# Optimization experiments

Hardware: AMD Instinct MI355X
Metric: run time of the kernel (lower is better)

Reference implementation:

```python
import jax, jax.numpy as jnp
import numpy as np

N, E, DIM, HEADS, EDGE_DIM = 50000, 800000, 128, 4, 1
C = DIM // HEADS  # per-head channels
EPS = 1e-5


def graph_ln(h, w, b):
    # PyG LayerNorm, mode='graph', batch=None: normalize over ALL nodes+features
    mu = h.mean()
    hc = h - mu
    std = jnp.sqrt(jnp.mean(hc * hc))
    return hc / (std + EPS) * w + b


def setup_inputs() -> dict:
    key = jax.random.key(0)
    ks = jax.random.split(key, 16)
    s = 1.0 / np.sqrt(DIM)
    return {
        "x": jax.random.normal(ks[0], (N, DIM), jnp.float32),
        "edge_index": jax.random.randint(ks[1], (2, E), 0, N, jnp.int32),
        "edge_weight": jax.random.uniform(ks[2], (E,), jnp.float32),
        "edge_attr": jax.random.normal(ks[3], (E, EDGE_DIM), jnp.float32),
        # GCNConv params
        "W_gcn": jax.random.normal(ks[4], (DIM, DIM), jnp.float32) * s,
        "b_gcn": jnp.zeros((DIM,), jnp.float32),
        # GATv2Conv params (share_weights=True -> single lin)
        "W_l": jax.random.normal(ks[5], (DIM, DIM), jnp.float32) * s,
        "b_l": jnp.zeros((DIM,), jnp.float32),
        "W_edge": jax.random.normal(ks[6], (EDGE_DIM, DIM), jnp.float32),
        "att": jax.random.normal(ks[7], (HEADS, C), jnp.float32) * (1.0 / np.sqrt(C)),
        "b_gat": jnp.zeros((DIM,), jnp.float32),
        # norms
        "gcn_nw": jnp.ones((DIM,), jnp.float32), "gcn_nb": jnp.zeros((DIM,), jnp.float32),
        "gat_nw": jnp.ones((DIM,), jnp.float32), "gat_nb": jnp.zeros((DIM,), jnp.float32),
        "out_nw": jnp.ones((DIM,), jnp.float32), "out_nb": jnp.zeros((DIM,), jnp.float32),
        "alpha": jnp.ones((2,), jnp.float32),
    }


def reference(x, edge_index, edge_weight, edge_attr, W_gcn, b_gcn, W_l, b_l,
              W_edge, att, b_gat, gcn_nw, gcn_nb, gat_nw, gat_nb, out_nw, out_nb, alpha):
    src, dst = edge_index[0], edge_index[1]

    # ---- GCN branch (normalize=True, add_self_loops=False) ----
    deg = jax.ops.segment_sum(edge_weight, dst, num_segments=N)
    dis = jnp.where(deg > 0, jax.lax.rsqrt(jnp.maximum(deg, 1e-30)), 0.0)
    norm = dis[src] * edge_weight * dis[dst]  # [E]
    xw = x @ W_gcn  # [N, DIM]
    h = jax.ops.segment_sum(norm[:, None] * xw[src], dst, num_segments=N) + b_gcn
    gcn_out = x + jax.nn.gelu(graph_ln(h, gcn_nw, gcn_nb), approximate=False)

    # ---- GATv2 branch (share_weights=True, edge_dim=1) ----
    xl = (x @ W_l + b_l).reshape(N, HEADS, C)
    e = (edge_attr @ W_edge).reshape(E, HEADS, C)
    z = jax.nn.leaky_relu(xl[dst] + xl[src] + e, negative_slope=0.2)  # [E,H,C]
    logits = jnp.einsum('ehc,hc->eh', z, att)  # [E,H]
    m = jax.ops.segment_max(logits, dst, num_segments=N)  # [N,H]
    a = jnp.exp(logits - m[dst])
    denom = jax.ops.segment_sum(a, dst, num_segments=N)
    a = a / (denom[dst] + 1e-16)  # softmax over incoming edges per dst, per head
    msg = xl[src] * a[:, :, None]  # [E,H,C]
    g = jax.ops.segment_sum(msg, dst, num_segments=N).reshape(N, DIM) + b_gat
    gat_out = x + jax.nn.gelu(graph_ln(g, gat_nw, gat_nb), approximate=False)

    # ---- fuse ----
    w = jax.nn.softmax(alpha)
    fused = w[0] * gcn_out + w[1] * gat_out
    return jax.nn.gelu(graph_ln(fused, out_nw, out_nb), approximate=False)
```

## Files before the change

kernel.cpp:

```cpp
#include <hip/hip_runtime.h>
#include <math.h>

#define DIM 128
#define HEADS 4
#define EPS 1e-5f
#define NBLK 1024

__device__ __forceinline__ float us2f(unsigned short u) {
  union { unsigned int i; float f; } c; c.i = ((unsigned int)u) << 16; return c.f;
}
__device__ __forceinline__ unsigned short f2us(float f) {
  union { float ff; unsigned int i; } c; c.ff = f;
  return (unsigned short)((c.i + 0x7FFFu + ((c.i >> 16) & 1u)) >> 16);
}
__device__ __forceinline__ float ldf(const void* p, size_t i, int fl32) {
  return fl32 ? ((const float*)p)[i] : us2f(((const unsigned short*)p)[i]);
}
__device__ __forceinline__ float gelu_exact(float v) {
  return 0.5f * v * (1.0f + erff(v * 0.7071067811865475f));
}
__device__ __forceinline__ int imin(int a, int b) { return a < b ? a : b; }

__device__ __forceinline__ int packed_pos(int c) { return ((c & ~1) << 1) | (c & 1); }

__global__ void __launch_bounds__(256)
k_detect(const unsigned short* __restrict__ x, long n, int* __restrict__ dflag) {
  long lim = n < 8192 ? n : 8192;
  int bad = 0;
  for (long i = threadIdx.x; i < lim; i += 256) {
    float v = us2f(x[i]);
    float a = fabsf(v);
    if (!(a == 0.0f || (a > 1e-30f && a < 1e3f))) bad++;
  }
  __shared__ int sb[256];
  sb[threadIdx.x] = bad;
  __syncthreads();
  for (int off = 128; off > 0; off >>= 1) {
    if ((int)threadIdx.x < off) sb[threadIdx.x] += sb[threadIdx.x + off];
    __syncthreads();
  }
  if (threadIdx.x == 0) dflag[0] = (sb[0] > 32) ? 1 : 0;
}

__global__ void k_deg_cnt(const int* __restrict__ dst, const void* __restrict__ ew,
                          float* __restrict__ deg, int* __restrict__ cnt,
                          int* __restrict__ rank, int E, const int* __restrict__ df) {
  const int fl32 = *df;
  int e = blockIdx.x * blockDim.x + threadIdx.x;
  if (e < E) {
    int d = dst[e];
    rank[e] = atomicAdd(&cnt[d], 1);
    float w = ldf(ew, e, fl32);
    if (isfinite(w)) atomicAdd(&deg[d], w);
  }
}

__global__ void k_dis(float* __restrict__ deg, int N) {
  int i = blockIdx.x * blockDim.x + threadIdx.x;
  if (i < N) {
    float d = deg[i];
    deg[i] = (d > 0.0f) ? rsqrtf(fmaxf(d, 1e-30f)) : 0.0f;
  }
}

__global__ void __launch_bounds__(256)
k_scan(const int* __restrict__ cnt, int* __restrict__ off, int N, int E) {
  __shared__ int part[256];
  int t = threadIdx.x;
  int chunk = (N + 255) / 256;
  int lo = t * chunk;
  int hi = lo + chunk; if (hi > N) hi = N;
  int s = 0;
  for (int i = lo; i < hi; ++i) s += cnt[i];
  part[t] = s;
  __syncthreads();
  if (t == 0) {
    int run = 0;
    for (int j = 0; j < 256; ++j) { int tmp = part[j]; part[j] = run; run += tmp; }
  }
  __syncthreads();
  int run = part[t];
  for (int i = lo; i < hi; ++i) { off[i] = run; run += cnt[i]; }
  if (t == 0) off[N] = E;
}

__global__ void k_scatter(const int* __restrict__ src, const int* __restrict__ dst,
                          const void* __restrict__ ew, const void* __restrict__ ea,
                          const float* __restrict__ dis, const int* __restrict__ off,
                          const int* __restrict__ rank, int4* __restrict__ csr,
                          int E, const int* __restrict__ df) {
  const int fl32 = *df;
  int e = blockIdx.x * blockDim.x + threadIdx.x;
  if (e >= E) return;
  int d = dst[e], s = src[e];
  int pos = off[d] + rank[e];
  float nm = dis[s] * ldf(ew, e, fl32) * dis[d];
  if (!isfinite(nm)) nm = 0.0f;
  float eav = ldf(ea, e, fl32);
  if (!isfinite(eav)) eav = 0.0f;
  csr[pos] = make_int4(s, __float_as_int(nm), __float_as_int(eav), 0);
}

__global__ void __launch_bounds__(256)
k_wprep(const void* __restrict__ Wg, const void* __restrict__ Wl,
        const void* __restrict__ bl, unsigned short* __restrict__ Bhi,
        unsigned short* __restrict__ Blo, float* __restrict__ bias2,
        const int* __restrict__ df) {
  const int fl32 = *df;
  int g = blockIdx.x * 256 + threadIdx.x;
  int col = g >> 7, k = g & 127;
  int t4 = col >> 2, r = col & 3;
  int wcol = t4 * 2 + (r & 1);
  float v = (r < 2) ? ldf(Wl, (size_t)k * DIM + wcol, fl32)
                    : ldf(Wg, (size_t)k * DIM + wcol, fl32);
  unsigned short hi = f2us(v);
  float lo = v - us2f(hi);
  Bhi[(size_t)col * 128 + k] = hi;
  Blo[(size_t)col * 128 + k] = f2us(lo);
  if (blockIdx.x == 0) {
    int c2 = threadIdx.x;
    int tt = c2 >> 2, rr = c2 & 3;
    bias2[c2] = (rr < 2) ? ldf(bl, tt * 2 + rr, fl32) : 0.0f;
  }
}

typedef __attribute__((ext_vector_type(8))) short short8v;
typedef __attribute__((ext_vector_type(4))) float f32x4;

__global__ void __launch_bounds__(256)
k_gemm_mfma(const void* __restrict__ x, const unsigned short* __restrict__ Bhi,
            const unsigned short* __restrict__ Blo, const float* __restrict__ bias2,
            unsigned short* __restrict__ packed, int N, const int* __restrict__ df) {
  const int fl32 = *df;
  __shared__ unsigned short Ahi[64 * 128];
  __shared__ unsigned short Alo[64 * 128];
  const int tid = threadIdx.x;
  const int r0 = blockIdx.x * 64;
  #pragma unroll
  for (int it = 0; it < 8; ++it) {
    int i4 = tid + it * 256;
    int row = i4 >> 5, kq = i4 & 31;
    int grow = r0 + row;
    float v0 = 0.f, v1 = 0.f, v2 = 0.f, v3 = 0.f;
    if (grow < N) {
      if (fl32) {
        float4 f = ((const float4*)x)[(size_t)grow * 32 + kq];
        v0 = f.x; v1 = f.y; v2 = f.z; v3 = f.w;
      } else {
        ushort4 u = ((const ushort4*)x)[(size_t)grow * 32 + kq];
        v0 = us2f(u.x); v1 = us2f(u.y); v2 = us2f(u.z); v3 = us2f(u.w);
      }
    }
    ushort4 hi = make_ushort4(f2us(v0), f2us(v1), f2us(v2), f2us(v3));
    ushort4 lo = make_ushort4(f2us(v0 - us2f(hi.x)), f2us(v1 - us2f(hi.y)),
                              f2us(v2 - us2f(hi.z)), f2us(v3 - us2f(hi.w)));
    int ba = (row * 256 + kq * 8) ^ ((row & 7) << 4);
    *(ushort4*)((char*)Ahi + ba) = hi;
    *(ushort4*)((char*)Alo + ba) = lo;
  }
  __syncthreads();
  const int lane = tid & 63, wid = tid >> 6;
  const int mbase = (wid >> 1) * 32;
  const int nbase = (wid & 1) * 128;
  const int lr = lane & 15, lk = lane >> 4;
  short8v ah[2][4], al[2][4];
  #pragma unroll
  for (int m = 0; m < 2; ++m) {
    #pragma unroll
    for (int ks = 0; ks < 4; ++ks) {
      int row = mbase + m * 16 + lr;
      int ba = (row * 256 + ks * 64 + lk * 16) ^ ((row & 7) << 4);
      ah[m][ks] = *(const short8v*)((const char*)Ahi + ba);
      al[m][ks] = *(const short8v*)((const char*)Alo + ba);
    }
  }
  f32x4 acc[2][8];
  const f32x4 zero = {0.0f, 0.0f, 0.0f, 0.0f};
  #pragma unroll
  for (int m = 0; m < 2; ++m)
    #pragma unroll
    for (int n = 0; n < 8; ++n) acc[m][n] = zero;
  #pragma unroll
  for (int n = 0; n < 8; ++n) {
    int col = nbase + n * 16 + lr;
    const unsigned short* bh0 = Bhi + (size_t)col * 128 + lk * 8;
    const unsigned short* bl0 = Blo + (size_t)col * 128 + lk * 8;
    #pragma unroll
    for (int ks = 0; ks < 4; ++ks) {
      short8v bh  = *(const short8v*)(bh0 + ks * 32);
      short8v blv = *(const short8v*)(bl0 + ks * 32);
      acc[0][n] = __builtin_amdgcn_mfma_f32_16x16x32_bf16(ah[0][ks], bh, acc[0][n], 0, 0, 0);
      acc[1][n] = __builtin_amdgcn_mfma_f32_16x16x32_bf16(ah[1][ks], bh, acc[1][n], 0, 0, 0);
      acc[0][n] = __builtin_amdgcn_mfma_f32_16x16x32_bf16(al[0][ks], bh, acc[0][n], 0, 0, 0);
      acc[1][n] = __builtin_amdgcn_mfma_f32_16x16x32_bf16(al[1][ks], bh, acc[1][n], 0, 0, 0);
      acc[0][n] = __builtin_amdgcn_mfma_f32_16x16x32_bf16(ah[0][ks], blv, acc[0][n], 0, 0, 0);
      acc[1][n] = __builtin_amdgcn_mfma_f32_16x16x32_bf16(ah[1][ks], blv, acc[1][n], 0, 0, 0);
    }
  }
  #pragma unroll
  for (int m = 0; m < 2; ++m) {
    #pragma unroll
    for (int n = 0; n < 8; ++n) {
      int col = nbase + n * 16 + lr;
      float bv = bias2[col];
      int rb = r0 + mbase + m * 16 + lk * 4;
      #pragma unroll
      for (int j = 0; j < 4; ++j) {
        int row = rb + j;
        if (row < N) {
          float v = acc[m][n][j] + bv;
          if (!isfinite(v)) v = 0.0f;
          packed[(size_t)row * 256 + col] = f2us(v);
        }
      }
    }
  }
}

#define GATHER(sidx) (*(const ushort4*)(packed + (size_t)(sidx) * 256 + lane * 4))

#define PROC(v, m) {                                                       \
  float nm = __int_as_float((m).y), eav = __int_as_float((m).z);           \
  float vx = us2f((v).x), vy = us2f((v).y);                                \
  float z0 = xd0 + vx + eav * wd0; z0 = (z0 > 0.f) ? z0 : 0.2f * z0;       \
  float z1 = xd1 + vy + eav * wd1; z1 = (z1 > 0.f) ? z1 : 0.2f * z1;       \
  float dt = z0 * at0 + z1 * at1;                                          \
  dt += __shfl_xor(dt, 1);                                                 \
  dt += __shfl_xor(dt, 2);                                                 \
  dt += __shfl_xor(dt, 4);                                                 \
  dt += __shfl_xor(dt, 8);                                                 \
  float e = __expf(-fabsf(dt - mx));                                       \
  bool up = dt > mx;                                                       \
  float corr = up ? e : 1.0f;                                              \
  float w = up ? 1.0f : e;                                                 \
  mx = up ? dt : mx;                                                       \
  den = fmaf(den, corr, w);                                                \
  ga0 = fmaf(ga0, corr, w * vx);                                           \
  ga1 = fmaf(ga1, corr, w * vy);                                           \
  hc0 = fmaf(nm, us2f((v).z), hc0);                                        \
  hc1 = fmaf(nm, us2f((v).w), hc1);                                        \
}

__global__ void __launch_bounds__(256)
k_mega(const int* __restrict__ off, const int4* __restrict__ csr,
       const unsigned short* __restrict__ packed,
       const void* __restrict__ Wed, const void* __restrict__ att,
       const void* __restrict__ bgcn, const void* __restrict__ bgat,
       float* __restrict__ h, float* __restrict__ g,
       double* __restrict__ pA, double* __restrict__ pB, int N,
       const int* __restrict__ df) {
  const int fl32 = *df;
  const int wid = threadIdx.x >> 6;
  const int lane = threadIdx.x & 63;
  const int n0 = blockIdx.x * 4;
  const int node = n0 + wid;
  const int c0 = lane * 2;
  float wd0 = ldf(Wed, c0, fl32), wd1 = ldf(Wed, c0 + 1, fl32);
  float at0 = ldf(att, c0, fl32), at1 = ldf(att, c0 + 1, fl32);

  const int blkBeg = off[n0];
  const int nTop = (n0 + 4 < N) ? (n0 + 4) : N;
  const int blkEnd = off[nTop];

  int beg = 0, end = 0;
  float xd0 = 0.f, xd1 = 0.f;
  if (node < N) {
    beg = off[node]; end = off[node + 1];
    ushort4 xd = *(const ushort4*)(packed + (size_t)node * 256 + lane * 4);
    xd0 = us2f(xd.x); xd1 = us2f(xd.y);
  }
  float mx = -INFINITY, den = 0.f;
  float ga0 = 0.f, ga1 = 0.f, hc0 = 0.f, hc1 = 0.f;

  __shared__ int4 smeta[256];

  for (int base = blkBeg; base < blkEnd; base += 256) {
    int wlen = blkEnd - base; if (wlen > 256) wlen = 256;
    __syncthreads();
    if ((int)threadIdx.x < wlen) smeta[threadIdx.x] = csr[base + (int)threadIdx.x];
    __syncthreads();
    int lo = beg > base ? beg : base;
    int hiEnd = base + wlen;
    int hi = end < hiEnd ? end : hiEnd;
    int cnt = hi - lo;
    if (cnt > 0) {
      int s0 = lo - base;
      int last = s0 + cnt - 1;
      ushort4 v0, v1, v2, v3, v4, v5, v6, v7;
      v0 = GATHER(smeta[imin(s0 + 0, last)].x);
      v1 = GATHER(smeta[imin(s0 + 1, last)].x);
      v2 = GATHER(smeta[imin(s0 + 2, last)].x);
      v3 = GATHER(smeta[imin(s0 + 3, last)].x);
      v4 = GATHER(smeta[imin(s0 + 4, last)].x);
      v5 = GATHER(smeta[imin(s0 + 5, last)].x);
      v6 = GATHER(smeta[imin(s0 + 6, last)].x);
      v7 = GATHER(smeta[imin(s0 + 7, last)].x);
      int i = 0;
      for (; i + 8 <= cnt; i += 8) {
        int4 m;
        m = smeta[s0 + i + 0]; PROC(v0, m); v0 = GATHER(smeta[imin(s0 + i + 8,  last)].x);
        m = smeta[s0 + i + 1]; PROC(v1, m); v1 = GATHER(smeta[imin(s0 + i + 9,  last)].x);
        m = smeta[s0 + i + 2]; PROC(v2, m); v2 = GATHER(smeta[imin(s0 + i + 10, last)].x);
        m = smeta[s0 + i + 3]; PROC(v3, m); v3 = GATHER(smeta[imin(s0 + i + 11, last)].x);
        m = smeta[s0 + i + 4]; PROC(v4, m); v4 = GATHER(smeta[imin(s0 + i + 12, last)].x);
        m = smeta[s0 + i + 5]; PROC(v5, m); v5 = GATHER(smeta[imin(s0 + i + 13, last)].x);
        m = smeta[s0 + i + 6]; PROC(v6, m); v6 = GATHER(smeta[imin(s0 + i + 14, last)].x);
        m = smeta[s0 + i + 7]; PROC(v7, m); v7 = GATHER(smeta[imin(s0 + i + 15, last)].x);
      }
      if (i < cnt) { int4 m = smeta[s0 + i]; PROC(v0, m); ++i; }
      if (i < cnt) { int4 m = smeta[s0 + i]; PROC(v1, m); ++i; }
      if (i < cnt) { int4 m = smeta[s0 + i]; PROC(v2, m); ++i; }
      if (i < cnt) { int4 m = smeta[s0 + i]; PROC(v3, m); ++i; }
      if (i < cnt) { int4 m = smeta[s0 + i]; PROC(v4, m); ++i; }
      if (i < cnt) { int4 m = smeta[s0 + i]; PROC(v5, m); ++i; }
      if (i < cnt) { int4 m = smeta[s0 + i]; PROC(v6, m); ++i; }
    }
  }

  double sA = 0.0, sA2 = 0.0, sB = 0.0, sB2 = 0.0;
  if (node < N) {
    float inv = (end > beg) ? 1.0f / (den + 1e-16f) : 0.0f;
    ga0 *= inv; ga1 *= inv;
    if (!isfinite(ga0)) ga0 = 0.0f;
    if (!isfinite(ga1)) ga1 = 0.0f;
    if (!isfinite(hc0)) hc0 = 0.0f;
    if (!isfinite(hc1)) hc1 = 0.0f;
    *(float2*)(h + (size_t)node * DIM + c0) = make_float2(hc0, hc1);
    *(float2*)(g + (size_t)node * DIM + c0) = make_float2(ga0, ga1);
    float hA0 = hc0 + ldf(bgcn, c0, fl32), hA1 = hc1 + ldf(bgcn, c0 + 1, fl32);
    float gB0 = ga0 + ldf(bgat, c0, fl32), gB1 = ga1 + ldf(bgat, c0 + 1, fl32);
    sA  = (double)hA0 + (double)hA1;
    sA2 = (double)hA0 * hA0 + (double)hA1 * hA1;
    sB  = (double)gB0 + (double)gB1;
    sB2 = (double)gB0 * gB0 + (double)gB1 * gB1;
  }
  __shared__ double l1[256], l2[256], l3[256], l4[256];
  l1[threadIdx.x] = sA; l2[threadIdx.x] = sA2; l3[threadIdx.x] = sB; l4[threadIdx.x] = sB2;
  __syncthreads();
  for (int o = 128; o > 0; o >>= 1) {
    if ((int)threadIdx.x < o) {
      l1[threadIdx.x] += l1[threadIdx.x + o];
      l2[threadIdx.x] += l2[threadIdx.x + o];
      l3[threadIdx.x] += l3[threadIdx.x + o];
      l4[threadIdx.x] += l4[threadIdx.x + o];
    }
    __syncthreads();
  }
  if (threadIdx.x == 0) {
    pA[2 * blockIdx.x] = l1[0]; pA[2 * blockIdx.x + 1] = l2[0];
    pB[2 * blockIdx.x] = l3[0]; pB[2 * blockIdx.x + 1] = l4[0];
  }
}

__device__ __forceinline__ void ln_params(double S, double S2, double M, float* mu_out, float* sc_out) {
  double mu = S / M;
  double v = S2 / M - mu * mu;
  if (!(v > 0.0)) v = 0.0;
  float fmu = (float)mu;
  float sc = 1.0f / ((float)sqrt(v) + EPS);
  if (!isfinite(fmu)) fmu = 0.0f;
  if (!isfinite(sc)) sc = 0.0f;
  *mu_out = fmu; *sc_out = sc;
}

__global__ void __launch_bounds__(256)
k_fin12(const double* __restrict__ pA, const double* __restrict__ pB, int nblk,
        const void* __restrict__ alpha, float* __restrict__ params, double M,
        const int* __restrict__ df) {
  const int fl32 = *df;
  __shared__ double l1[256], l2[256], l3[256], l4[256];
  double a = 0, b = 0, c = 0, d = 0;
  for (int j = threadIdx.x; j < nblk; j += 256) {
    a += pA[2 * j]; b += pA[2 * j + 1];
    c += pB[2 * j]; d += pB[2 * j + 1];
  }
  l1[threadIdx.x] = a; l2[threadIdx.x] = b; l3[threadIdx.x] = c; l4[threadIdx.x] = d;
  __syncthreads();
  for (int off = 128; off > 0; off >>= 1) {
    if ((int)threadIdx.x < off) {
      l1[threadIdx.x] += l1[threadIdx.x + off];
      l2[threadIdx.x] += l2[threadIdx.x + off];
      l3[threadIdx.x] += l3[threadIdx.x + off];
      l4[threadIdx.x] += l4[threadIdx.x + off];
    }
    __syncthreads();
  }
  if (threadIdx.x == 0) {
    ln_params(l1[0], l2[0], M, &params[0], &params[1]);
    ln_params(l3[0], l4[0], M, &params[2], &params[3]);
    float a0 = ldf(alpha, 0, fl32), a1 = ldf(alpha, 1, fl32);
    if (!isfinite(a0)) a0 = 0.0f;
    if (!isfinite(a1)) a1 = 0.0f;
    float mx = fmaxf(a0, a1);
    float e0 = expf(a0 - mx), e1 = expf(a1 - mx);
    float inv = 1.0f / (e0 + e1);
    params[4] = e0 * inv;
    params[5] = e1 * inv;
  }
}

__global__ void __launch_bounds__(256)
k_fin3(const double* __restrict__ pC, float* __restrict__ params, double M) {
  __shared__ double l1[256], l2[256];
  double a = 0, b = 0;
  for (int j = threadIdx.x; j < NBLK; j += 256) { a += pC[2 * j]; b += pC[2 * j + 1]; }
  l1[threadIdx.x] = a; l2[threadIdx.x] = b;
  __syncthreads();
  for (int off = 128; off > 0; off >>= 1) {
    if ((int)threadIdx.x < off) {
      l1[threadIdx.x] += l1[threadIdx.x + off];
      l2[threadIdx.x] += l2[threadIdx.x + off];
    }
    __syncthreads();
  }
  if (threadIdx.x == 0) ln_params(l1[0], l2[0], M, &params[6], &params[7]);
}

__global__ void __launch_bounds__(256)
k_fuse(const void* __restrict__ x, float* h, const float* __restrict__ g,
       const void* __restrict__ b_gcn, const void* __restrict__ b_gat,
       const void* __restrict__ gcn_nw, const void* __restrict__ gcn_nb,
       const void* __restrict__ gat_nw, const void* __restrict__ gat_nb,
       const float* __restrict__ params, double* __restrict__ pC, long n4,
       const int* __restrict__ df) {
  const int fl32 = *df;
  float mu1 = params[0], sc1 = params[1], mu2 = params[2], sc2 = params[3];
  float w0 = params[4], w1 = params[5];
  double s = 0.0, s2 = 0.0;
  long stride = (long)gridDim.x * blockDim.x;
  for (long i4 = (long)blockIdx.x * blockDim.x + threadIdx.x; i4 < n4; i4 += stride) {
    int c = (int)((i4 * 4) & (DIM - 1));
    float4 hv4 = ((const float4*)h)[i4];
    float4 gv4 = ((const float4*)g)[i4];
    float xv[4];
    if (fl32) {
      float4 xf = ((const float4*)x)[i4];
      xv[0] = xf.x; xv[1] = xf.y; xv[2] = xf.z; xv[3] = xf.w;
    } else {
      ushort4 xu = ((const ushort4*)x)[i4];
      xv[0] = us2f(xu.x); xv[1] = us2f(xu.y); xv[2] = us2f(xu.z); xv[3] = us2f(xu.w);
    }
    float hv[4] = {hv4.x, hv4.y, hv4.z, hv4.w};
    float gv[4] = {gv4.x, gv4.y, gv4.z, gv4.w};
    float fo[4];
    #pragma unroll
    for (int j = 0; j < 4; ++j) {
      int cj = c + j;
      float hb = hv[j] + ldf(b_gcn, cj, fl32);
      float gb = gv[j] + ldf(b_gat, cj, fl32);
      float go = xv[j] + gelu_exact((hb - mu1) * sc1 * ldf(gcn_nw, cj, fl32) + ldf(gcn_nb, cj, fl32));
      float ao = xv[j] + gelu_exact((gb - mu2) * sc2 * ldf(gat_nw, cj, fl32) + ldf(gat_nb, cj, fl32));
      float f = w0 * go + w1 * ao;
      if (!isfinite(f)) f = 0.0f;
      fo[j] = f;
      s += f; s2 += (double)f * f;
    }
    ((float4*)h)[i4] = make_float4(fo[0], fo[1], fo[2], fo[3]);
  }
  __shared__ double ls[256], ls2[256];
  ls[threadIdx.x] = s; ls2[threadIdx.x] = s2;
  __syncthreads();
  for (int off = 128; off > 0; off >>= 1) {
    if ((int)threadIdx.x < off) {
      ls[threadIdx.x] += ls[threadIdx.x + off];
      ls2[threadIdx.x] += ls2[threadIdx.x + off];
    }
    __syncthreads();
  }
  if (threadIdx.x == 0) { pC[2 * blockIdx.x] = ls[0]; pC[2 * blockIdx.x + 1] = ls2[0]; }
}

__global__ void k_final(const float* __restrict__ fused, const void* __restrict__ nw,
                        const void* __restrict__ nb, const float* __restrict__ params,
                        void* __restrict__ out, long n4, const int* __restrict__ df) {
  const int fl32 = *df;
  long i4 = (long)blockIdx.x * blockDim.x + threadIdx.x;
  if (i4 >= n4) return;
  int c = (int)((i4 * 4) & (DIM - 1));
  float mu = params[6], sc = params[7];
  float4 f4 = ((const float4*)fused)[i4];
  float fv[4] = {f4.x, f4.y, f4.z, f4.w};
  float rv[4];
  #pragma unroll
  for (int j = 0; j < 4; ++j) {
    int cj = c + j;
    float r = gelu_exact((fv[j] - mu) * sc * ldf(nw, cj, fl32) + ldf(nb, cj, fl32));
    if (!isfinite(r)) r = 0.0f;
    rv[j] = r;
  }
  if (fl32) {
    ((float4*)out)[i4] = make_float4(rv[0], rv[1], rv[2], rv[3]);
  } else {
    ((ushort4*)out)[i4] = make_ushort4(f2us(rv[0]), f2us(rv[1]), f2us(rv[2]), f2us(rv[3]));
  }
}

extern "C" void kernel_launch(void* const* d_in, const int* in_sizes, int n_in,
                              void* d_out, int out_size, void* d_ws, size_t ws_size,
                              hipStream_t stream) {
  const void* x    = d_in[0];
  const int*  ei   = (const int*)d_in[1];
  const void* ew   = d_in[2];
  const void* ea   = d_in[3];
  const void* Wg   = d_in[4];
  const void* bgcn = d_in[5];
  const void* Wl   = d_in[6];
  const void* bl   = d_in[7];
  const void* Wed  = d_in[8];
  const void* att  = d_in[9];
  const void* bgat = d_in[10];
  const void* gcn_nw = d_in[11];
  const void* gcn_nb = d_in[12];
  const void* gat_nw = d_in[13];
  const void* gat_nb = d_in[14];
  const void* out_nw = d_in[15];
  const void* out_nb = d_in[16];
  const void* alpha  = d_in[17];

  const int N = in_sizes[0] / DIM;
  const int E = in_sizes[2];
  const int* src  = ei;
  const int* dstp = ei + E;
  const size_t ND = (size_t)N * DIM;
  const int nAgg = (N + 3) / 4;

  char* ws = (char*)d_ws;
  size_t o = 0;
  auto alloc = [&](size_t bytes) { size_t r = o; o += (bytes + 255) & ~(size_t)255; return r; };
  size_t o_deg    = alloc((size_t)N * 4);
  size_t o_cnt    = alloc((size_t)N * 4);
  size_t zero_end = o;
  size_t o_off    = alloc((size_t)(N + 1) * 4);
  size_t o_h      = alloc(ND * 4);
  size_t o_g      = alloc(ND * 4);
  size_t o_packed = alloc(ND * 4);
  size_t o_csr    = alloc((size_t)E * 16);
  size_t o_par    = alloc(8 * 4);
  size_t o_pA     = alloc((size_t)nAgg * 2 * 8);
  size_t o_pB     = alloc((size_t)nAgg * 2 * 8);
  size_t o_pC     = alloc((size_t)NBLK * 2 * 8);
  size_t o_flag   = alloc(4);
  size_t o_bh     = alloc((size_t)256 * 128 * 2);
  size_t o_blo    = alloc((size_t)256 * 128 * 2);
  size_t o_b2     = alloc((size_t)256 * 4);
  (void)ws_size; (void)n_in; (void)out_size;

  float* deg     = (float*)(ws + o_deg);
  int*   cnt     = (int*)(ws + o_cnt);
  int*   off     = (int*)(ws + o_off);
  float* h       = (float*)(ws + o_h);
  int*   rank    = (int*)(ws + o_h);
  float* g       = (float*)(ws + o_g);
  unsigned short* packed = (unsigned short*)(ws + o_packed);
  int4*  csr     = (int4*)(ws + o_csr);
  float* params  = (float*)(ws + o_par);
  double* pA     = (double*)(ws + o_pA);
  double* pB     = (double*)(ws + o_pB);
  double* pC     = (double*)(ws + o_pC);
  int* dflag     = (int*)(ws + o_flag);
  unsigned short* Bhi = (unsigned short*)(ws + o_bh);
  unsigned short* Blo = (unsigned short*)(ws + o_blo);
  float* bias2   = (float*)(ws + o_b2);

  hipMemsetAsync(ws, 0, zero_end, stream);
  k_detect<<<1, 256, 0, stream>>>((const unsigned short*)x, (long)ND, dflag);

  k_wprep<<<128, 256, 0, stream>>>(Wg, Wl, bl, Bhi, Blo, bias2, dflag);

  int ebk = (E + 255) / 256;
  k_deg_cnt<<<ebk, 256, 0, stream>>>(dstp, ew, deg, cnt, rank, E, dflag);
  k_dis<<<(N + 255) / 256, 256, 0, stream>>>(deg, N);
  k_scan<<<1, 256, 0, stream>>>(cnt, off, N, E);
  k_scatter<<<ebk, 256, 0, stream>>>(src, dstp, ew, ea, deg, off, rank, csr, E, dflag);

  k_gemm_mfma<<<(N + 63) / 64, 256, 0, stream>>>(x, Bhi, Blo, bias2, packed, N, dflag);

  k_mega<<<nAgg, 256, 0, stream>>>(off, csr, packed, Wed, att, bgcn, bgat,
                                   h, g, pA, pB, N, dflag);

  k_fin12<<<1, 256, 0, stream>>>(pA, pB, nAgg, alpha, params, (double)ND, dflag);

  const long n4 = (long)(ND / 4);
  k_fuse<<<NBLK, 256, 0, stream>>>(x, h, g, bgcn, bgat, gcn_nw, gcn_nb, gat_nw, gat_nb,
                                   params, pC, n4, dflag);
  k_fin3<<<1, 256, 0, stream>>>(pC, params, (double)ND);
  k_final<<<(int)((n4 + 255) / 256), 256, 0, stream>>>(h, out_nw, out_nb, params,
                                                       d_out, n4, dflag);
}
```

Measured before the change: 531.3 us.

## Process four edges per wavefront in GAT/GCN aggregation with online-softmax merge

The per-destination aggregation kernel now splits each 64-lane wavefront into four 16-lane groups. Each group handles a different incoming edge, loading 32-byte slices of the packed row per lane. Per-group online-softmax state is merged across groups with cross-lane shuffles at the end, which cuts the dot-product shuffle reduction from four steps to two and adds more independent gathers in flight. The GEMM also skips the bf16 low-part correction MFMAs when the input is not fp32. This adds extra register pressure and a final merge step, and uses shallower explicit prefetch (three slots instead of eight).

```diff
diff --git a/kernel.cpp b/kernel.cpp
--- a/kernel.cpp
+++ b/kernel.cpp
@@ -126,6 +126,7 @@
 
 typedef __attribute__((ext_vector_type(8))) short short8v;
 typedef __attribute__((ext_vector_type(4))) float f32x4;
+typedef __attribute__((ext_vector_type(8))) unsigned short u16x8;
 
 __global__ void __launch_bounds__(256)
 k_gemm_mfma(const void* __restrict__ x, const unsigned short* __restrict__ Bhi,
@@ -180,21 +181,35 @@
   for (int m = 0; m < 2; ++m)
     #pragma unroll
     for (int n = 0; n < 8; ++n) acc[m][n] = zero;
-  #pragma unroll
-  for (int n = 0; n < 8; ++n) {
-    int col = nbase + n * 16 + lr;
-    const unsigned short* bh0 = Bhi + (size_t)col * 128 + lk * 8;
-    const unsigned short* bl0 = Blo + (size_t)col * 128 + lk * 8;
-    #pragma unroll
-    for (int ks = 0; ks < 4; ++ks) {
-      short8v bh  = *(const short8v*)(bh0 + ks * 32);
-      short8v blv = *(const short8v*)(bl0 + ks * 32);
-      acc[0][n] = __builtin_amdgcn_mfma_f32_16x16x32_bf16(ah[0][ks], bh, acc[0][n], 0, 0, 0);
-      acc[1][n] = __builtin_amdgcn_mfma_f32_16x16x32_bf16(ah[1][ks], bh, acc[1][n], 0, 0, 0);
-      acc[0][n] = __builtin_amdgcn_mfma_f32_16x16x32_bf16(al[0][ks], bh, acc[0][n], 0, 0, 0);
-      acc[1][n] = __builtin_amdgcn_mfma_f32_16x16x32_bf16(al[1][ks], bh, acc[1][n], 0, 0, 0);
-      acc[0][n] = __builtin_amdgcn_mfma_f32_16x16x32_bf16(ah[0][ks], blv, acc[0][n], 0, 0, 0);
-      acc[1][n] = __builtin_amdgcn_mfma_f32_16x16x32_bf16(ah[1][ks], blv, acc[1][n], 0, 0, 0);
+  if (fl32) {
+    #pragma unroll
+    for (int n = 0; n < 8; ++n) {
+      int col = nbase + n * 16 + lr;
+      const unsigned short* bh0 = Bhi + (size_t)col * 128 + lk * 8;
+      const unsigned short* bl0 = Blo + (size_t)col * 128 + lk * 8;
+      #pragma unroll
+      for (int ks = 0; ks < 4; ++ks) {
+        short8v bh  = *(const short8v*)(bh0 + ks * 32);
+        short8v blv = *(const short8v*)(bl0 + ks * 32);
+        acc[0][n] = __builtin_amdgcn_mfma_f32_16x16x32_bf16(ah[0][ks], bh, acc[0][n], 0, 0, 0);
+        acc[1][n] = __builtin_amdgcn_mfma_f32_16x16x32_bf16(ah[1][ks], bh, acc[1][n], 0, 0, 0);
+        acc[0][n] = __builtin_amdgcn_mfma_f32_16x16x32_bf16(al[0][ks], bh, acc[0][n], 0, 0, 0);
+        acc[1][n] = __builtin_amdgcn_mfma_f32_16x16x32_bf16(al[1][ks], bh, acc[1][n], 0, 0, 0);
+        acc[0][n] = __builtin_amdgcn_mfma_f32_16x16x32_bf16(ah[0][ks], blv, acc[0][n], 0, 0, 0);
+        acc[1][n] = __builtin_amdgcn_mfma_f32_16x16x32_bf16(ah[1][ks], blv, acc[1][n], 0, 0, 0);
+      }
+    }
+  } else {
+    #pragma unroll
+    for (int n = 0; n < 8; ++n) {
+      int col = nbase + n * 16 + lr;
+      const unsigned short* bh0 = Bhi + (size_t)col * 128 + lk * 8;
+      #pragma unroll
+      for (int ks = 0; ks < 4; ++ks) {
+        short8v bh = *(const short8v*)(bh0 + ks * 32);
+        acc[0][n] = __builtin_amdgcn_mfma_f32_16x16x32_bf16(ah[0][ks], bh, acc[0][n], 0, 0, 0);
+        acc[1][n] = __builtin_amdgcn_mfma_f32_16x16x32_bf16(ah[1][ks], bh, acc[1][n], 0, 0, 0);
+      }
     }
   }
   #pragma unroll
@@ -217,28 +232,47 @@
   }
 }
 
-#define GATHER(sidx) (*(const ushort4*)(packed + (size_t)(sidx) * 256 + lane * 4))
-
-#define PROC(v, m) {                                                       \
-  float nm = __int_as_float((m).y), eav = __int_as_float((m).z);           \
-  float vx = us2f((v).x), vy = us2f((v).y);                                \
-  float z0 = xd0 + vx + eav * wd0; z0 = (z0 > 0.f) ? z0 : 0.2f * z0;       \
-  float z1 = xd1 + vy + eav * wd1; z1 = (z1 > 0.f) ? z1 : 0.2f * z1;       \
-  float dt = z0 * at0 + z1 * at1;                                          \
-  dt += __shfl_xor(dt, 1);                                                 \
-  dt += __shfl_xor(dt, 2);                                                 \
-  dt += __shfl_xor(dt, 4);                                                 \
-  dt += __shfl_xor(dt, 8);                                                 \
-  float e = __expf(-fabsf(dt - mx));                                       \
-  bool up = dt > mx;                                                       \
-  float corr = up ? e : 1.0f;                                              \
-  float w = up ? 1.0f : e;                                                 \
-  mx = up ? dt : mx;                                                       \
-  den = fmaf(den, corr, w);                                                \
-  ga0 = fmaf(ga0, corr, w * vx);                                           \
-  ga1 = fmaf(ga1, corr, w * vy);                                           \
-  hc0 = fmaf(nm, us2f((v).z), hc0);                                        \
-  hc1 = fmaf(nm, us2f((v).w), hc1);                                        \
+#define MPRE(M, VA, VB, i) {                                                  \
+  int eidx_ = imin(s0 + (i) + grp, last);                                     \
+  M = smeta[eidx_];                                                           \
+  const unsigned short* rp_ = packed + (size_t)M.x * 256 + sl * 16;           \
+  VA = *(const u16x8*)rp_;                                                    \
+  VB = *(const u16x8*)(rp_ + 8);                                              \
+}
+
+#define MPROC(M, VA, VB, i) {                                                 \
+  bool valid = ((i) + grp) < cnt;                                             \
+  float nm = valid ? __int_as_float((M).y) : 0.0f;                            \
+  float eav = __int_as_float((M).z);                                          \
+  float xl0 = us2f((VA)[0]), xl1 = us2f((VA)[1]);                             \
+  float xl2 = us2f((VA)[4]), xl3 = us2f((VA)[5]);                             \
+  float xl4 = us2f((VB)[0]), xl5 = us2f((VB)[1]);                             \
+  float xl6 = us2f((VB)[4]), xl7 = us2f((VB)[5]);                             \
+  float z, dt;                                                                \
+  z = xd[0] + xl0 + eav * wd[0]; z = (z > 0.f) ? z : 0.2f * z; dt  = z * at[0]; \
+  z = xd[1] + xl1 + eav * wd[1]; z = (z > 0.f) ? z : 0.2f * z; dt += z * at[1]; \
+  z = xd[2] + xl2 + eav * wd[2]; z = (z > 0.f) ? z : 0.2f * z; dt += z * at[2]; \
+  z = xd[3] + xl3 + eav * wd[3]; z = (z > 0.f) ? z : 0.2f * z; dt += z * at[3]; \
+  z = xd[4] + xl4 + eav * wd[4]; z = (z > 0.f) ? z : 0.2f * z; dt += z * at[4]; \
+  z = xd[5] + xl5 + eav * wd[5]; z = (z > 0.f) ? z : 0.2f * z; dt += z * at[5]; \
+  z = xd[6] + xl6 + eav * wd[6]; z = (z > 0.f) ? z : 0.2f * z; dt += z * at[6]; \
+  z = xd[7] + xl7 + eav * wd[7]; z = (z > 0.f) ? z : 0.2f * z; dt += z * at[7]; \
+  dt += __shfl_xor(dt, 1);                                                    \
+  dt += __shfl_xor(dt, 2);                                                    \
+  float e = __expf(-fabsf(dt - mx));                                          \
+  bool up = (dt > mx) && valid;                                               \
+  float corr = up ? e : 1.0f;                                                 \
+  float w = valid ? (up ? 1.0f : e) : 0.0f;                                   \
+  mx = up ? dt : mx;                                                          \
+  den = fmaf(den, corr, w);                                                   \
+  ga[0] = fmaf(ga[0], corr, w * xl0); ga[1] = fmaf(ga[1], corr, w * xl1);     \
+  ga[2] = fmaf(ga[2], corr, w * xl2); ga[3] = fmaf(ga[3], corr, w * xl3);     \
+  ga[4] = fmaf(ga[4], corr, w * xl4); ga[5] = fmaf(ga[5], corr, w * xl5);     \
+  ga[6] = fmaf(ga[6], corr, w * xl6); ga[7] = fmaf(ga[7], corr, w * xl7);     \
+  hc[0] = fmaf(nm, us2f((VA)[2]), hc[0]); hc[1] = fmaf(nm, us2f((VA)[3]), hc[1]); \
+  hc[2] = fmaf(nm, us2f((VA)[6]), hc[2]); hc[3] = fmaf(nm, us2f((VA)[7]), hc[3]); \
+  hc[4] = fmaf(nm, us2f((VB)[2]), hc[4]); hc[5] = fmaf(nm, us2f((VB)[3]), hc[5]); \
+  hc[6] = fmaf(nm, us2f((VB)[6]), hc[6]); hc[7] = fmaf(nm, us2f((VB)[7]), hc[7]); \
 }
 
 __global__ void __launch_bounds__(256)
@@ -252,25 +286,37 @@
   const int fl32 = *df;
   const int wid = threadIdx.x >> 6;
   const int lane = threadIdx.x & 63;
+  const int grp = lane >> 4;
+  const int sl = lane & 15;
+  const int c0 = sl * 8;
   const int n0 = blockIdx.x * 4;
   const int node = n0 + wid;
-  const int c0 = lane * 2;
-  float wd0 = ldf(Wed, c0, fl32), wd1 = ldf(Wed, c0 + 1, fl32);
-  float at0 = ldf(att, c0, fl32), at1 = ldf(att, c0 + 1, fl32);
+
+  float wd[8], at[8], xd[8];
+  #pragma unroll
+  for (int j = 0; j < 8; ++j) {
+    wd[j] = ldf(Wed, c0 + j, fl32);
+    at[j] = ldf(att, c0 + j, fl32);
+    xd[j] = 0.f;
+  }
 
   const int blkBeg = off[n0];
   const int nTop = (n0 + 4 < N) ? (n0 + 4) : N;
   const int blkEnd = off[nTop];
 
   int beg = 0, end = 0;
-  float xd0 = 0.f, xd1 = 0.f;
   if (node < N) {
     beg = off[node]; end = off[node + 1];
-    ushort4 xd = *(const ushort4*)(packed + (size_t)node * 256 + lane * 4);
-    xd0 = us2f(xd.x); xd1 = us2f(xd.y);
+    const unsigned short* rp = packed + (size_t)node * 256 + sl * 16;
+    u16x8 da = *(const u16x8*)rp;
+    u16x8 db = *(const u16x8*)(rp + 8);
+    xd[0] = us2f(da[0]); xd[1] = us2f(da[1]); xd[2] = us2f(da[4]); xd[3] = us2f(da[5]);
+    xd[4] = us2f(db[0]); xd[5] = us2f(db[1]); xd[6] = us2f(db[4]); xd[7] = us2f(db[5]);
   }
   float mx = -INFINITY, den = 0.f;
-  float ga0 = 0.f, ga1 = 0.f, hc0 = 0.f, hc1 = 0.f;
+  float ga[8], hc[8];
+  #pragma unroll
+  for (int j = 0; j < 8; ++j) { ga[j] = 0.f; hc[j] = 0.f; }
 
   __shared__ int4 smeta[256];
 
@@ -283,56 +329,65 @@
     int hiEnd = base + wlen;
     int hi = end < hiEnd ? end : hiEnd;
     int cnt = hi - lo;
-    if (cnt > 0) {
-      int s0 = lo - base;
-      int last = s0 + cnt - 1;
-      ushort4 v0, v1, v2, v3, v4, v5, v6, v7;
-      v0 = GATHER(smeta[imin(s0 + 0, last)].x);
-      v1 = GATHER(smeta[imin(s0 + 1, last)].x);
-      v2 = GATHER(smeta[imin(s0 + 2, last)].x);
-      v3 = GATHER(smeta[imin(s0 + 3, last)].x);
-      v4 = GATHER(smeta[imin(s0 + 4, last)].x);
-      v5 = GATHER(smeta[imin(s0 + 5, last)].x);
-      v6 = GATHER(smeta[imin(s0 + 6, last)].x);
-      v7 = GATHER(smeta[imin(s0 + 7, last)].x);
-      int i = 0;
-      for (; i + 8 <= cnt; i += 8) {
-        int4 m;
-        m = smeta[s0 + i + 0]; PROC(v0, m); v0 = GATHER(smeta[imin(s0 + i + 8,  last)].x);
-        m = smeta[s0 + i + 1]; PROC(v1, m); v1 = GATHER(smeta[imin(s0 + i + 9,  last)].x);
-        m = smeta[s0 + i + 2]; PROC(v2, m); v2 = GATHER(smeta[imin(s0 + i + 10, last)].x);
-        m = smeta[s0 + i + 3]; PROC(v3, m); v3 = GATHER(smeta[imin(s0 + i + 11, last)].x);
-        m = smeta[s0 + i + 4]; PROC(v4, m); v4 = GATHER(smeta[imin(s0 + i + 12, last)].x);
-        m = smeta[s0 + i + 5]; PROC(v5, m); v5 = GATHER(smeta[imin(s0 + i + 13, last)].x);
-        m = smeta[s0 + i + 6]; PROC(v6, m); v6 = GATHER(smeta[imin(s0 + i + 14, last)].x);
-        m = smeta[s0 + i + 7]; PROC(v7, m); v7 = GATHER(smeta[imin(s0 + i + 15, last)].x);
-      }
-      if (i < cnt) { int4 m = smeta[s0 + i]; PROC(v0, m); ++i; }
-      if (i < cnt) { int4 m = smeta[s0 + i]; PROC(v1, m); ++i; }
-      if (i < cnt) { int4 m = smeta[s0 + i]; PROC(v2, m); ++i; }
-      if (i < cnt) { int4 m = smeta[s0 + i]; PROC(v3, m); ++i; }
-      if (i < cnt) { int4 m = smeta[s0 + i]; PROC(v4, m); ++i; }
-      if (i < cnt) { int4 m = smeta[s0 + i]; PROC(v5, m); ++i; }
-      if (i < cnt) { int4 m = smeta[s0 + i]; PROC(v6, m); ++i; }
-    }
+    if (cnt <= 0) continue;
+    int s0 = lo - base;
+    int last = s0 + cnt - 1;
+    int4 mA, mB, mC;
+    u16x8 vaA, vbA, vaB, vbB, vaC, vbC;
+    MPRE(mA, vaA, vbA, 0);
+    MPRE(mB, vaB, vbB, 4);
+    MPRE(mC, vaC, vbC, 8);
+    int i = 0;
+    while (true) {
+      MPROC(mA, vaA, vbA, i);
+      MPRE(mA, vaA, vbA, i + 12);
+      i += 4; if (i >= cnt) break;
+      MPROC(mB, vaB, vbB, i);
+      MPRE(mB, vaB, vbB, i + 12);
+      i += 4; if (i >= cnt) break;
+      MPROC(mC, vaC, vbC, i);
+      MPRE(mC, vaC, vbC, i + 12);
+      i += 4; if (i >= cnt) break;
+    }
+  }
+
+  #pragma unroll
+  for (int r = 16; r <= 32; r <<= 1) {
+    float mo = __shfl_xor(mx, r);
+    float dn = __shfl_xor(den, r);
+    float M = fmaxf(mx, mo);
+    float f1 = (mx == M) ? 1.0f : __expf(mx - M);
+    float f2 = (mo == M) ? 1.0f : __expf(mo - M);
+    den = den * f1 + dn * f2;
+    #pragma unroll
+    for (int j = 0; j < 8; ++j) {
+      float go = __shfl_xor(ga[j], r);
+      ga[j] = ga[j] * f1 + go * f2;
+      hc[j] += __shfl_xor(hc[j], r);
+    }
+    mx = M;
   }
 
   double sA = 0.0, sA2 = 0.0, sB = 0.0, sB2 = 0.0;
-  if (node < N) {
+  if (node < N && grp == 0) {
     float inv = (end > beg) ? 1.0f / (den + 1e-16f) : 0.0f;
-    ga0 *= inv; ga1 *= inv;
-    if (!isfinite(ga0)) ga0 = 0.0f;
-    if (!isfinite(ga1)) ga1 = 0.0f;
-    if (!isfinite(hc0)) hc0 = 0.0f;
-    if (!isfinite(hc1)) hc1 = 0.0f;
-    *(float2*)(h + (size_t)node * DIM + c0) = make_float2(hc0, hc1);
-    *(float2*)(g + (size_t)node * DIM + c0) = make_float2(ga0, ga1);
-    float hA0 = hc0 + ldf(bgcn, c0, fl32), hA1 = hc1 + ldf(bgcn, c0 + 1, fl32);
-    float gB0 = ga0 + ldf(bgat, c0, fl32), gB1 = ga1 + ldf(bgat, c0 + 1, fl32);
-    sA  = (double)hA0 + (double)hA1;
-    sA2 = (double)hA0 * hA0 + (double)hA1 * hA1;
-    sB  = (double)gB0 + (double)gB1;
-    sB2 = (double)gB0 * gB0 + (double)gB1 * gB1;
+    #pragma unroll
+    for (int j = 0; j < 8; ++j) {
+      ga[j] *= inv;
+      if (!isfinite(ga[j])) ga[j] = 0.0f;
+      if (!isfinite(hc[j])) hc[j] = 0.0f;
+    }
+    *(float4*)(h + (size_t)node * DIM + c0)     = make_float4(hc[0], hc[1], hc[2], hc[3]);
+    *(float4*)(h + (size_t)node * DIM + c0 + 4) = make_float4(hc[4], hc[5], hc[6], hc[7]);
+    *(float4*)(g + (size_t)node * DIM + c0)     = make_float4(ga[0], ga[1], ga[2], ga[3]);
+    *(float4*)(g + (size_t)node * DIM + c0 + 4) = make_float4(ga[4], ga[5], ga[6], ga[7]);
+    #pragma unroll
+    for (int j = 0; j < 8; ++j) {
+      float hA = hc[j] + ldf(bgcn, c0 + j, fl32);
+      float gB = ga[j] + ldf(bgat, c0 + j, fl32);
+      sA += hA; sA2 += (double)hA * hA;
+      sB += gB; sB2 += (double)gB * gB;
+    }
   }
   __shared__ double l1[256], l2[256], l3[256], l4[256];
   l1[threadIdx.x] = sA; l2[threadIdx.x] = sA2; l3[threadIdx.x] = sB; l4[threadIdx.x] = sB2;
```

New measurement: 603.8 us. +13.6%, slower.

## Compute degree from CSR instead of float atomics; skip lo-split MFMA for bf16

Applied to the files above, without the earlier changes.

Degree accumulation no longer uses float atomicAdd per edge. The scatter now stores the raw weight and the dst index in the CSR. A per-node kernel then sums the weights from the CSR segments, and a separate per-edge pass computes the normalization in place. The GEMM skips the hi/lo split MFMAs when the input is bf16, and the fuse block count is doubled. This adds two kernel launches and an extra pass over the CSR in exchange for removing the contended float atomics.

```diff
diff --git a/kernel.cpp b/kernel.cpp
--- a/kernel.cpp
+++ b/kernel.cpp
@@ -4,7 +4,7 @@
 #define DIM 128
 #define HEADS 4
 #define EPS 1e-5f
-#define NBLK 1024
+#define NBLK 2048
 
 __device__ __forceinline__ float us2f(unsigned short u) {
   union { unsigned int i; float f; } c; c.i = ((unsigned int)u) << 16; return c.f;
@@ -42,25 +42,10 @@
   if (threadIdx.x == 0) dflag[0] = (sb[0] > 32) ? 1 : 0;
 }
 
-__global__ void k_deg_cnt(const int* __restrict__ dst, const void* __restrict__ ew,
-                          float* __restrict__ deg, int* __restrict__ cnt,
-                          int* __restrict__ rank, int E, const int* __restrict__ df) {
-  const int fl32 = *df;
+__global__ void k_cnt(const int* __restrict__ dst, int* __restrict__ cnt,
+                      int* __restrict__ rank, int E) {
   int e = blockIdx.x * blockDim.x + threadIdx.x;
-  if (e < E) {
-    int d = dst[e];
-    rank[e] = atomicAdd(&cnt[d], 1);
-    float w = ldf(ew, e, fl32);
-    if (isfinite(w)) atomicAdd(&deg[d], w);
-  }
-}
-
-__global__ void k_dis(float* __restrict__ deg, int N) {
-  int i = blockIdx.x * blockDim.x + threadIdx.x;
-  if (i < N) {
-    float d = deg[i];
-    deg[i] = (d > 0.0f) ? rsqrtf(fmaxf(d, 1e-30f)) : 0.0f;
-  }
+  if (e < E) rank[e] = atomicAdd(&cnt[dst[e]], 1);
 }
 
 __global__ void __launch_bounds__(256)
@@ -86,19 +71,39 @@
 
 __global__ void k_scatter(const int* __restrict__ src, const int* __restrict__ dst,
                           const void* __restrict__ ew, const void* __restrict__ ea,
-                          const float* __restrict__ dis, const int* __restrict__ off,
-                          const int* __restrict__ rank, int4* __restrict__ csr,
-                          int E, const int* __restrict__ df) {
+                          const int* __restrict__ off, const int* __restrict__ rank,
+                          int4* __restrict__ csr, int E, const int* __restrict__ df) {
   const int fl32 = *df;
   int e = blockIdx.x * blockDim.x + threadIdx.x;
   if (e >= E) return;
   int d = dst[e], s = src[e];
   int pos = off[d] + rank[e];
-  float nm = dis[s] * ldf(ew, e, fl32) * dis[d];
-  if (!isfinite(nm)) nm = 0.0f;
+  float w = ldf(ew, e, fl32);
   float eav = ldf(ea, e, fl32);
   if (!isfinite(eav)) eav = 0.0f;
-  csr[pos] = make_int4(s, __float_as_int(nm), __float_as_int(eav), 0);
+  csr[pos] = make_int4(s, __float_as_int(w), __float_as_int(eav), d);
+}
+
+__global__ void k_degdis(const int* __restrict__ off, const int4* __restrict__ csr,
+                         float* __restrict__ dis, int N) {
+  int i = blockIdx.x * blockDim.x + threadIdx.x;
+  if (i >= N) return;
+  int b = off[i], t = off[i + 1];
+  float s = 0.f;
+  for (int j = b; j < t; ++j) {
+    float w = __int_as_float(csr[j].y);
+    if (isfinite(w)) s += w;
+  }
+  dis[i] = (s > 0.0f) ? rsqrtf(fmaxf(s, 1e-30f)) : 0.0f;
+}
+
+__global__ void k_nm(int4* __restrict__ csr, const float* __restrict__ dis, int E) {
+  int e = blockIdx.x * blockDim.x + threadIdx.x;
+  if (e >= E) return;
+  int4 c = csr[e];
+  float nm = dis[c.x] * __int_as_float(c.y) * dis[c.w];
+  if (!isfinite(nm)) nm = 0.0f;
+  ((int*)&csr[e])[1] = __float_as_int(nm);
 }
 
 __global__ void __launch_bounds__(256)
@@ -180,21 +185,35 @@
   for (int m = 0; m < 2; ++m)
     #pragma unroll
     for (int n = 0; n < 8; ++n) acc[m][n] = zero;
-  #pragma unroll
-  for (int n = 0; n < 8; ++n) {
-    int col = nbase + n * 16 + lr;
-    const unsigned short* bh0 = Bhi + (size_t)col * 128 + lk * 8;
-    const unsigned short* bl0 = Blo + (size_t)col * 128 + lk * 8;
+  if (fl32) {
     #pragma unroll
-    for (int ks = 0; ks < 4; ++ks) {
-      short8v bh  = *(const short8v*)(bh0 + ks * 32);
-      short8v blv = *(const short8v*)(bl0 + ks * 32);
-      acc[0][n] = __builtin_amdgcn_mfma_f32_16x16x32_bf16(ah[0][ks], bh, acc[0][n], 0, 0, 0);
-      acc[1][n] = __builtin_amdgcn_mfma_f32_16x16x32_bf16(ah[1][ks], bh, acc[1][n], 0, 0, 0);
-      acc[0][n] = __builtin_amdgcn_mfma_f32_16x16x32_bf16(al[0][ks], bh, acc[0][n], 0, 0, 0);
-      acc[1][n] = __builtin_amdgcn_mfma_f32_16x16x32_bf16(al[1][ks], bh, acc[1][n], 0, 0, 0);
-      acc[0][n] = __builtin_amdgcn_mfma_f32_16x16x32_bf16(ah[0][ks], blv, acc[0][n], 0, 0, 0);
-      acc[1][n] = __builtin_amdgcn_mfma_f32_16x16x32_bf16(ah[1][ks], blv, acc[1][n], 0, 0, 0);
+    for (int n = 0; n < 8; ++n) {
+      int col = nbase + n * 16 + lr;
+      const unsigned short* bh0 = Bhi + (size_t)col * 128 + lk * 8;
+      const unsigned short* bl0 = Blo + (size_t)col * 128 + lk * 8;
+      #pragma unroll
+      for (int ks = 0; ks < 4; ++ks) {
+        short8v bh  = *(const short8v*)(bh0 + ks * 32);
+        short8v blv = *(const short8v*)(bl0 + ks * 32);
+        acc[0][n] = __builtin_amdgcn_mfma_f32_16x16x32_bf16(ah[0][ks], bh, acc[0][n], 0, 0, 0);
+        acc[1][n] = __builtin_amdgcn_mfma_f32_16x16x32_bf16(ah[1][ks], bh, acc[1][n], 0, 0, 0);
+        acc[0][n] = __builtin_amdgcn_mfma_f32_16x16x32_bf16(al[0][ks], bh, acc[0][n], 0, 0, 0);
+        acc[1][n] = __builtin_amdgcn_mfma_f32_16x16x32_bf16(al[1][ks], bh, acc[1][n], 0, 0, 0);
+        acc[0][n] = __builtin_amdgcn_mfma_f32_16x16x32_bf16(ah[0][ks], blv, acc[0][n], 0, 0, 0);
+        acc[1][n] = __builtin_amdgcn_mfma_f32_16x16x32_bf16(ah[1][ks], blv, acc[1][n], 0, 0, 0);
+      }
+    }
+  } else {
+    #pragma unroll
+    for (int n = 0; n < 8; ++n) {
+      int col = nbase + n * 16 + lr;
+      const unsigned short* bh0 = Bhi + (size_t)col * 128 + lk * 8;
+      #pragma unroll
+      for (int ks = 0; ks < 4; ++ks) {
+        short8v bh = *(const short8v*)(bh0 + ks * 32);
+        acc[0][n] = __builtin_amdgcn_mfma_f32_16x16x32_bf16(ah[0][ks], bh, acc[0][n], 0, 0, 0);
+        acc[1][n] = __builtin_amdgcn_mfma_f32_16x16x32_bf16(ah[1][ks], bh, acc[1][n], 0, 0, 0);
+      }
     }
   }
   #pragma unroll
@@ -545,7 +564,7 @@
   size_t o_b2     = alloc((size_t)256 * 4);
   (void)ws_size; (void)n_in; (void)out_size;
 
-  float* deg     = (float*)(ws + o_deg);
+  float* dis     = (float*)(ws + o_deg);
   int*   cnt     = (int*)(ws + o_cnt);
   int*   off     = (int*)(ws + o_off);
   float* h       = (float*)(ws + o_h);
@@ -568,10 +587,11 @@
   k_wprep<<<128, 256, 0, stream>>>(Wg, Wl, bl, Bhi, Blo, bias2, dflag);
 
   int ebk = (E + 255) / 256;
-  k_deg_cnt<<<ebk, 256, 0, stream>>>(dstp, ew, deg, cnt, rank, E, dflag);
-  k_dis<<<(N + 255) / 256, 256, 0, stream>>>(deg, N);
+  k_cnt<<<ebk, 256, 0, stream>>>(dstp, cnt, rank, E);
   k_scan<<<1, 256, 0, stream>>>(cnt, off, N, E);
-  k_scatter<<<ebk, 256, 0, stream>>>(src, dstp, ew, ea, deg, off, rank, csr, E, dflag);
+  k_scatter<<<ebk, 256, 0, stream>>>(src, dstp, ew, ea, off, rank, csr, E, dflag);
+  k_degdis<<<(N + 255) / 256, 256, 0, stream>>>(off, csr, dis, N);
+  k_nm<<<ebk, 256, 0, stream>>>(csr, dis, E);
 
   k_gemm_mfma<<<(N + 63) / 64, 256, 0, stream>>>(x, Bhi, Blo, bias2, packed, N, dflag);
 
```

After: 510.3 us. -4.0%, faster.
